# Kernel optimization log

Measured on AMD Instinct MI355X. Metric: run time of the kernel, lower is better.

The kernel has to match this reference:

```python
import jax, jax.numpy as jnp
import numpy as np

H, C = 2, 32  # heads, out_channels per head
NEG_SLOPE = 0.2


def gatv2_layer(h, src, dst, ea, W, b, We, att, bias, N):
    # shared lin_l = lin_r (share_weights=True)
    z = (h @ W + b).reshape(N, H, C)                      # [N,H,C]
    e = (ea @ We).reshape(-1, H, C)                        # [E',H,C]
    s = jax.nn.leaky_relu(z[dst] + z[src] + e, NEG_SLOPE)  # [E',H,C]
    alpha = jnp.einsum('ehc,hc->eh', s, att)               # [E',H]
    # segment softmax over destination neighborhoods
    m = jax.ops.segment_max(alpha, dst, num_segments=N)
    m = jnp.where(jnp.isfinite(m), m, 0.0)
    ex = jnp.exp(alpha - m[dst])
    denom = jax.ops.segment_sum(ex, dst, num_segments=N)
    a = ex / (denom[dst] + 1e-16)                          # [E',H]
    msg = (z[src] * a[:, :, None]).reshape(-1, H * C)      # [E',H*C]
    out = jax.ops.segment_sum(msg, dst, num_segments=N) + bias
    return out                                             # [N,H*C]


def setup_inputs() -> dict:
    key = jax.random.key(0)
    ks = jax.random.split(key, 16)
    N, E = 50000, 800000
    inp = {
        'x': jax.random.normal(ks[0], (N, 2), jnp.float32),
        'edge_index': jax.random.randint(ks[1], (2, E), 0, N, jnp.int64 if jax.config.jax_enable_x64 else jnp.int32).astype(jnp.int32),
        'edge_attr': jax.random.uniform(ks[2], (E, 2), jnp.float32),
        'dest_index': 123,
        'W0': jax.random.normal(ks[3], (2, 64), jnp.float32) * 0.5,
        'b0': jnp.zeros((64,), jnp.float32),
        'We0': jax.random.normal(ks[4], (2, 64), jnp.float32) * 0.5,
        'att0': jax.random.normal(ks[5], (H, C), jnp.float32) * 0.5,
        'bias0': jnp.zeros((64,), jnp.float32),
        'W1': jax.random.normal(ks[6], (64, 64), jnp.float32) * 0.125,
        'b1': jnp.zeros((64,), jnp.float32),
        'We1': jax.random.normal(ks[7], (2, 64), jnp.float32) * 0.5,
        'att1': jax.random.normal(ks[8], (H, C), jnp.float32) * 0.5,
        'bias1': jnp.zeros((64,), jnp.float32),
        'Wm1': jax.random.normal(ks[9], (194, 32), jnp.float32) * 0.07,
        'bm1': jnp.zeros((32,), jnp.float32),
        'Wm2': jax.random.normal(ks[10], (32, 1), jnp.float32) * 0.17,
        'bm2': jnp.zeros((1,), jnp.float32),
    }
    return inp


def reference(x, edge_index, edge_attr, dest_index,
              W0, b0, We0, att0, bias0,
              W1, b1, We1, att1, bias1,
              Wm1, bm1, Wm2, bm2):
    N = x.shape[0]
    # add self loops (fill_value='mean' for edge_attr)
    loops = jnp.arange(N, dtype=edge_index.dtype)
    src = jnp.concatenate([edge_index[0], loops])
    dst = jnp.concatenate([edge_index[1], loops])
    ea_sl = jnp.concatenate(
        [edge_attr, jnp.broadcast_to(edge_attr.mean(axis=0), (N, edge_attr.shape[1]))], axis=0)

    h = x
    h = jax.nn.elu(gatv2_layer(h, src, dst, ea_sl, W0, b0, We0, att0, bias0, N))
    h = jax.nn.elu(gatv2_layer(h, src, dst, ea_sl, W1, b1, We1, att1, bias1, N))

    goal = h[dest_index]                                   # [64]
    src_emb = h[edge_index[0]]                             # [E,64]
    dst_emb = h[edge_index[1]]                             # [E,64]
    goal_rep = jnp.broadcast_to(goal, (edge_index.shape[1], goal.shape[0]))
    edge_in = jnp.concatenate([src_emb, dst_emb, goal_rep, edge_attr], axis=-1)  # [E,194]
    hmlp = jax.nn.relu(edge_in @ Wm1 + bm1)
    logits = (hmlp @ Wm2 + bm2).squeeze(-1)                # [E]
    return logits
```

## Files before the change

### kernel.cpp

```cpp
#include <hip/hip_runtime.h>
#include <hip/hip_bf16.h>
#include <hip/hip_fp16.h>
#include <math.h>


typedef __attribute__((ext_vector_type(8))) short short8;
typedef __attribute__((ext_vector_type(4))) float f32x4;

#define BSH 6
#define CAP 2048
#define CH 4096

template <int IMM>
__device__ __forceinline__ float swz(float x) {
    return __int_as_float(__builtin_amdgcn_ds_swizzle(__float_as_int(x), IMM));
}

template <int CTRL>
__device__ __forceinline__ float dpp_add(float p) {
    int t = __builtin_amdgcn_update_dpp(0, __float_as_int(p), CTRL, 0xF, 0xF, true);
    return p + __int_as_float(t);
}

__device__ __forceinline__ short2 bsplit(float x) {
    unsigned u = __float_as_uint(x);
    short hi = (short)(u >> 16);
    float hif = __uint_as_float(u & 0xFFFF0000u);
    short lo = (short)(__float_as_uint(x - hif) >> 16);
    return make_short2(hi, lo);
}

__global__ __launch_bounds__(512) void setup_kernel(const float* __restrict__ W1,
                                                    const float* __restrict__ Wm1,
                                                    short* __restrict__ BfW1,
                                                    short* __restrict__ BfWm,
                                                    int* __restrict__ bucket_cursor,
                                                    float* __restrict__ easum, int nbuck) {
    if (blockIdx.x == 2) {
        for (int i = threadIdx.x; i < nbuck; i += 512) bucket_cursor[i] = i * CAP;
        if (threadIdx.x < 2) easum[threadIdx.x] = 0.f;
        return;
    }
    int snt = threadIdx.x >> 6;
    int lane = threadIdx.x & 63;
    int s = snt >> 2, nt = snt & 3;
    int col = nt * 16 + (lane & 15);
    short* Bf = blockIdx.x == 0 ? BfW1 : BfWm;
#pragma unroll
    for (int j = 0; j < 8; ++j) {
        int k = s * 32 + (lane >> 4) * 8 + j;
        float v;
        if (blockIdx.x == 0) {
            v = W1[k * 64 + col];
        } else {
            v = (col < 32) ? Wm1[k * 32 + col] : Wm1[(64 + k) * 32 + (col - 32)];
        }
        short2 t = bsplit(v);
        Bf[(snt * 2 + 0) * 512 + lane * 8 + j] = t.x;
        Bf[(snt * 2 + 1) * 512 + lane * 8 + j] = t.y;
    }
}

__global__ __launch_bounds__(256) void phaseA_kernel(const int* __restrict__ ei,
                                                     const float2* __restrict__ ea,
                                                     int* __restrict__ bucket_cursor,
                                                     float* __restrict__ easum,
                                                     float4* __restrict__ staged,
                                                     int E, int nbuck) {
    extern __shared__ int sm[];
    int* lcnt = sm;
    int* lbase = sm + nbuck;
    __shared__ float r0[4], r1[4];
    int tid = threadIdx.x;
    for (int i = tid; i < nbuck; i += 256) lcnt[i] = 0;
    __syncthreads();
    int base = blockIdx.x * CH;
    int end = min(base + CH, E);
    for (int i = base + tid; i < end; i += 256) {
        int d = ei[E + i];
        atomicAdd(&lcnt[d >> BSH], 1);
    }
    __syncthreads();
    for (int i = tid; i < nbuck; i += 256) {
        int c = lcnt[i];
        lbase[i] = c ? atomicAdd(&bucket_cursor[i], c) : 0;
        lcnt[i] = 0;
    }
    __syncthreads();
    float s0 = 0.f, s1 = 0.f;
    for (int i = base + tid; i < end; i += 256) {
        int s = ei[i], d = ei[E + i];
        float2 v = ea[i];
        s0 += v.x; s1 += v.y;
        int b = d >> BSH;
        int pos = lbase[b] + atomicAdd(&lcnt[b], 1);
        staged[pos] = make_float4(__int_as_float(s), v.x, v.y, __int_as_float(d));
    }
#pragma unroll
    for (int o = 32; o >= 1; o >>= 1) {
        s0 += __shfl_xor(s0, o);
        s1 += __shfl_xor(s1, o);
    }
    int wave = tid >> 6;
    if ((tid & 63) == 0) { r0[wave] = s0; r1[wave] = s1; }
    __syncthreads();
    if (tid == 0) {
        atomicAdd(&easum[0], r0[0] + r0[1] + r0[2] + r0[3]);
        atomicAdd(&easum[1], r1[0] + r1[1] + r1[2] + r1[3]);
    }
}

__global__ __launch_bounds__(512, 8) void phaseB_mega(
    const float4* __restrict__ staged, const int* __restrict__ bucket_cursor,
    const float* __restrict__ easum, const float2* __restrict__ x,
    const float* __restrict__ W0, const float* __restrict__ b0,
    const float* __restrict__ We, const float* __restrict__ att,
    const float* __restrict__ bias, const short* __restrict__ Bf,
    const float* __restrict__ b1,
    int* __restrict__ row_ptr, float4* __restrict__ recs,
    __half* __restrict__ z16, int N, int E, int nbuck) {
    __shared__ int cnt64[64];
    __shared__ int offs[64];
    __shared__ int psum8[8];
    __shared__ float acc6[64][6];
    __shared__ float h0s[64 * 64];
    int b = blockIdx.x;
    int n0g = b << BSH;
    int tid = threadIdx.x;
    int lane = tid & 63;
    int wave = tid >> 6;
    int local = 0;
    for (int j = tid; j < b; j += 512) local += bucket_cursor[j] - j * CAP;
#pragma unroll
    for (int o = 32; o >= 1; o >>= 1) local += __shfl_xor(local, o);
    if (tid < 64) cnt64[tid] = 0;
    for (int i = tid; i < 64 * 6; i += 512) ((float*)acc6)[i] = 0.f;
    if (lane == 0) psum8[wave] = local;
    __syncthreads();
    int bbase = 64 * b + psum8[0] + psum8[1] + psum8[2] + psum8[3]
                       + psum8[4] + psum8[5] + psum8[6] + psum8[7];
    int sbeg = b * CAP;
    int send = bucket_cursor[b];
    int nsl = send - sbeg;
    int nodes_here = min(64, N - n0g);
    int nrec = nsl + nodes_here;
    float invE = 1.f / (float)E;
    float m0 = easum[0] * invE, m1 = easum[1] * invE;

    {
        int sub = lane & 15;
        int eslot = lane >> 4;
        int ch0 = ((sub & 7) << 2) + ((sub >> 3) << 5);
        float Wx[4], Wy[4], bc[4], w0e[4], w1e[4], at[4];
#pragma unroll
        for (int j = 0; j < 4; ++j) {
            Wx[j] = W0[ch0 + j];  Wy[j] = W0[64 + ch0 + j];  bc[j] = b0[ch0 + j];
            w0e[j] = We[ch0 + j]; w1e[j] = We[64 + ch0 + j]; at[j] = att[ch0 + j];
        }
        int npass = (nsl + 3) >> 2;
        for (int p = wave; p < npass; p += 8) {
            int idx = p * 4 + eslot;
            bool valid = idx < nsl;
            float4 r = staged[sbeg + (valid ? idx : nsl - 1)];
            int s = __float_as_int(r.x);
            int d = __float_as_int(r.w);
            float2 xs = x[s];
            float2 xd = x[d];
            float P = 0.f;
#pragma unroll
            for (int j = 0; j < 4; ++j) {
                float zs = fmaf(xs.x, Wx[j], fmaf(xs.y, Wy[j], bc[j]));
                float zd = fmaf(xd.x, Wx[j], fmaf(xd.y, Wy[j], bc[j]));
                float t0 = zd + zs + fmaf(r.y, w0e[j], r.z * w1e[j]);
                t0 = fmaxf(t0, 0.2f * t0);
                P = fmaf(t0, at[j], P);
            }
            P += swz<0x041F>(P);
            P += swz<0x081F>(P);
            P += swz<0x101F>(P);
            float Po = swz<0x201F>(P);
            float Ph0 = (sub < 8) ? P : Po;
            float Ph1 = (sub < 8) ? Po : P;
            float w0 = __expf(fminf(Ph0, 60.f));
            float w1 = __expf(fminf(Ph1, 60.f));
            if (sub == 0 && valid) {
                int dl = d - n0g;
                atomicAdd(&acc6[dl][0], w0);
                atomicAdd(&acc6[dl][1], w0 * xs.x);
                atomicAdd(&acc6[dl][2], w0 * xs.y);
                atomicAdd(&acc6[dl][3], w1);
                atomicAdd(&acc6[dl][4], w1 * xs.x);
                atomicAdd(&acc6[dl][5], w1 * xs.y);
                atomicAdd(&cnt64[dl], 1);
            }
        }
    }
    __syncthreads();

    if (wave == 0) {
        int node = n0g + lane;
        int tot = cnt64[lane] + ((node < N) ? 1 : 0);
        int v = tot;
#pragma unroll
        for (int st = 1; st < 64; st <<= 1) {
            int u = __shfl_up(v, st);
            if (lane >= st) v += u;
        }
        if (node < N) {
            int excl = bbase + v - tot;
            row_ptr[node] = excl;
            recs[excl] = make_float4(__int_as_float(node), m0, m1, __int_as_float(node));
            offs[lane] = excl + 1;
        }
        if (b == nbuck - 1 && lane == 0) row_ptr[N] = bbase + nrec;
    }
    for (int k = 0; k < 8; ++k) {
        int q = wave + 8 * k;
        int ch = lane;
        int node = n0g + q;
        float hv = 0.f;
        if (node < N) {
            float2 xn = x[node];
            float W0c = W0[ch], W0c2 = W0[64 + ch], b0c = b0[ch];
            float zn = fmaf(xn.x, W0c, fmaf(xn.y, W0c2, b0c));
            float ts = fmaf(2.f, zn, fmaf(m0, We[ch], m1 * We[64 + ch]));
            ts = fmaxf(ts, 0.2f * ts);
            float p = ts * att[ch];
#pragma unroll
            for (int o = 1; o <= 16; o <<= 1) p += __shfl_xor(p, o);
            float wself = __expf(fminf(p, 60.f));
            int hsel = (ch >= 32) ? 3 : 0;
            float l  = acc6[q][hsel]     + wself;
            float Sx = acc6[q][hsel + 1] + wself * xn.x;
            float Sy = acc6[q][hsel + 2] + wself * xn.y;
            float num = fmaf(W0c, Sx, fmaf(W0c2, Sy, b0c * l));
            float v = num / (l + 1e-16f) + bias[ch];
            hv = (v > 0.f) ? v : expm1f(v);
        }
        h0s[q * 64 + ch] = hv;
    }
    __syncthreads();

    int m = lane & 15, quad = lane >> 4;
    int rowb = (wave & 3) * 16 + m;
    int ntb = (wave >> 2) * 2;
    f32x4 acc[2] = {{0.f, 0.f, 0.f, 0.f}, {0.f, 0.f, 0.f, 0.f}};
#pragma unroll
    for (int s = 0; s < 2; ++s) {
        const float* ap = h0s + rowb * 64 + s * 32 + quad * 8;
        float4 a0 = *(const float4*)ap;
        float4 a1 = *(const float4*)(ap + 4);
        short8 ahi, alo;
        short2 t;
        t = bsplit(a0.x); ahi[0] = t.x; alo[0] = t.y;
        t = bsplit(a0.y); ahi[1] = t.x; alo[1] = t.y;
        t = bsplit(a0.z); ahi[2] = t.x; alo[2] = t.y;
        t = bsplit(a0.w); ahi[3] = t.x; alo[3] = t.y;
        t = bsplit(a1.x); ahi[4] = t.x; alo[4] = t.y;
        t = bsplit(a1.y); ahi[5] = t.x; alo[5] = t.y;
        t = bsplit(a1.z); ahi[6] = t.x; alo[6] = t.y;
        t = bsplit(a1.w); ahi[7] = t.x; alo[7] = t.y;
#pragma unroll
        for (int u = 0; u < 2; ++u) {
            const short* bp = Bf + ((s * 4 + ntb + u) * 2) * 512 + lane * 8;
            short8 bhi = *(const short8*)bp;
            short8 blo = *(const short8*)(bp + 512);
            acc[u] = __builtin_amdgcn_mfma_f32_16x16x32_bf16(ahi, bhi, acc[u], 0, 0, 0);
            acc[u] = __builtin_amdgcn_mfma_f32_16x16x32_bf16(ahi, blo, acc[u], 0, 0, 0);
            acc[u] = __builtin_amdgcn_mfma_f32_16x16x32_bf16(alo, bhi, acc[u], 0, 0, 0);
        }
    }
#pragma unroll
    for (int u = 0; u < 2; ++u) {
        int col = (ntb + u) * 16 + m;
        float bj = b1[col];
#pragma unroll
        for (int r = 0; r < 4; ++r) {
            int orow = n0g + (wave & 3) * 16 + quad * 4 + r;
            if (orow < N) z16[(size_t)orow * 64 + col] = __float2half(acc[u][r] + bj);
        }
    }
    for (int i = sbeg + tid; i < send; i += 512) {
        float4 r = staged[i];
        int d = __float_as_int(r.w);
        int pos = atomicAdd(&offs[d - n0g], 1);
        recs[pos] = r;
    }
}

__global__ __launch_bounds__(256) void agg1_kernel(
    const __half* __restrict__ z, const int* __restrict__ row_ptr,
    const float4* __restrict__ recs,
    const float* __restrict__ We, const float* __restrict__ att,
    const float* __restrict__ bias, float* __restrict__ hout, int N) {
    int gtid = blockIdx.x * blockDim.x + threadIdx.x;
    int n = gtid >> 6;
    if (n >= N) return;
    n = __builtin_amdgcn_readfirstlane(n);
    int lane = threadIdx.x & 63;
    int half = lane >> 5;
    int c = (lane & 31) * 2;

    float We0a = We[c],      We0b = We[c + 1];
    float We1a = We[64 + c], We1b = We[64 + c + 1];
    float atta = att[c],     attb = att[c + 1];
    float2 znf = __half22float2(*(const __half2*)(z + (size_t)n * 64 + c));

    int beg = row_ptr[n], end = row_ptr[n + 1];
    float ll[4] = {0.f, 0.f, 0.f, 0.f};
    float a0[4] = {0.f, 0.f, 0.f, 0.f};
    float a1[4] = {0.f, 0.f, 0.f, 0.f};
    for (int i = beg; i < end; i += 8) {
        float w[4]; float2 zs[4];
#pragma unroll
        for (int k = 0; k < 4; ++k) {
            int idx = i + 2 * k + half;
            int idc = idx < end ? idx : end - 1;
            float4 r = recs[idc];
            int s = __float_as_int(r.x);
            zs[k] = __half22float2(*(const __half2*)(z + (size_t)s * 64 + c));
            float sj0 = znf.x + zs[k].x + fmaf(r.y, We0a, r.z * We1a);
            float sj1 = znf.y + zs[k].y + fmaf(r.y, We0b, r.z * We1b);
            sj0 = fmaxf(sj0, 0.2f * sj0);
            sj1 = fmaxf(sj1, 0.2f * sj1);
            float p = fmaf(sj0, atta, sj1 * attb);
            p = dpp_add<0xB1>(p);
            p = dpp_add<0x4E>(p);
            p = dpp_add<0x141>(p);
            p = dpp_add<0x140>(p);
            float ww = __expf(fminf(p, 60.f));
            w[k] = (idx < end) ? ww : 0.f;
        }
#pragma unroll
        for (int k = 0; k < 4; ++k) {
            ll[k] += w[k];
            a0[k] = fmaf(w[k], zs[k].x, a0[k]);
            a1[k] = fmaf(w[k], zs[k].y, a1[k]);
        }
    }
    float l  = (ll[0] + ll[1]) + (ll[2] + ll[3]);
    float s0 = (a0[0] + a0[1]) + (a0[2] + a0[3]);
    float s1 = (a1[0] + a1[1]) + (a1[2] + a1[3]);
    l  += __shfl_xor(l, 32);
    s0 += __shfl_xor(s0, 32);
    s1 += __shfl_xor(s1, 32);
    float inv = 1.f / (l + 1e-16f);
    float v0 = s0 * inv + bias[c];
    float v1 = s1 * inv + bias[c + 1];
    v0 = (v0 > 0.f) ? v0 : expm1f(v0);
    v1 = (v1 > 0.f) ? v1 : expm1f(v1);
    *(float2*)(hout + (size_t)n * 64 + c) = make_float2(v0, v1);
}

__global__ __launch_bounds__(256) void mfma_gemm64(const float* __restrict__ h,
                                                   const short* __restrict__ Bf,
                                                   __half* __restrict__ out, int N,
                                                   const float* __restrict__ Wm1,
                                                   const float* __restrict__ bm1,
                                                   const int* __restrict__ dest,
                                                   float* __restrict__ gv) {
    int wave = threadIdx.x >> 6;
    int lane = threadIdx.x & 63;
    int n0 = blockIdx.x * 64 + wave * 16;
    if (n0 < N) {
        int m = lane & 15, quad = lane >> 4;
        int arow = n0 + m;
        if (arow > N - 1) arow = N - 1;
        f32x4 acc[4] = {{0.f, 0.f, 0.f, 0.f}, {0.f, 0.f, 0.f, 0.f},
                        {0.f, 0.f, 0.f, 0.f}, {0.f, 0.f, 0.f, 0.f}};
#pragma unroll
        for (int s = 0; s < 2; ++s) {
            const float* ap = h + (size_t)arow * 64 + s * 32 + quad * 8;
            float4 a0 = *(const float4*)ap;
            float4 a1 = *(const float4*)(ap + 4);
            short8 ahi, alo;
            short2 t;
            t = bsplit(a0.x); ahi[0] = t.x; alo[0] = t.y;
            t = bsplit(a0.y); ahi[1] = t.x; alo[1] = t.y;
            t = bsplit(a0.z); ahi[2] = t.x; alo[2] = t.y;
            t = bsplit(a0.w); ahi[3] = t.x; alo[3] = t.y;
            t = bsplit(a1.x); ahi[4] = t.x; alo[4] = t.y;
            t = bsplit(a1.y); ahi[5] = t.x; alo[5] = t.y;
            t = bsplit(a1.z); ahi[6] = t.x; alo[6] = t.y;
            t = bsplit(a1.w); ahi[7] = t.x; alo[7] = t.y;
#pragma unroll
            for (int nt = 0; nt < 4; ++nt) {
                const short* bp = Bf + ((s * 4 + nt) * 2) * 512 + lane * 8;
                short8 bhi = *(const short8*)bp;
                short8 blo = *(const short8*)(bp + 512);
                acc[nt] = __builtin_amdgcn_mfma_f32_16x16x32_bf16(ahi, bhi, acc[nt], 0, 0, 0);
                acc[nt] = __builtin_amdgcn_mfma_f32_16x16x32_bf16(ahi, blo, acc[nt], 0, 0, 0);
                acc[nt] = __builtin_amdgcn_mfma_f32_16x16x32_bf16(alo, bhi, acc[nt], 0, 0, 0);
            }
        }
#pragma unroll
        for (int nt = 0; nt < 4; ++nt) {
            int col = nt * 16 + m;
#pragma unroll
            for (int r = 0; r < 4; ++r) {
                int orow = n0 + quad * 4 + r;
                if (orow < N) out[(size_t)orow * 64 + col] = __float2half(acc[nt][r]);
            }
        }
    }
    if (gv && blockIdx.x == 0 && threadIdx.x < 32) {
        int dd = dest[0];
        int q = threadIdx.x;
        float acc2 = bm1[q];
        for (int k = 0; k < 64; ++k)
            acc2 = fmaf(h[(size_t)dd * 64 + k], Wm1[(128 + k) * 32 + q], acc2);
        gv[q] = acc2;
    }
}

__global__ __launch_bounds__(256) void edge_mlp_kernel(
    const int* __restrict__ ei, const float2* __restrict__ ea,
    const __half* __restrict__ hsd, const float* __restrict__ gvec,
    const float* __restrict__ WrowA, const float* __restrict__ WrowB,
    const float* __restrict__ Wm2, const float* __restrict__ bm2,
    float* __restrict__ out, int E) {
    int tid = blockIdx.x * blockDim.x + threadIdx.x;
    int e = tid >> 3;
    int j = tid & 7;
    if (e >= E) return;
    int s = ei[e], d = ei[E + e];
    float2 eav = ea[e];
    const __half2* ps = (const __half2*)(hsd + (size_t)s * 64 + j * 4);
    const __half2* pd = (const __half2*)(hsd + (size_t)d * 64 + 32 + j * 4);
    float2 a01 = __half22float2(ps[0]), a23 = __half22float2(ps[1]);
    float2 b01 = __half22float2(pd[0]), b23 = __half22float2(pd[1]);
    float4 g = *(const float4*)(gvec + j * 4);
    float4 wa = *(const float4*)(WrowA + j * 4);
    float4 wb = *(const float4*)(WrowB + j * 4);
    float4 w2 = *(const float4*)(Wm2 + j * 4);
    float acc = 0.f, v;
    v = fmaf(eav.x, wa.x, fmaf(eav.y, wb.x, a01.x + b01.x + g.x)); v = fmaxf(v, 0.f); acc = fmaf(v, w2.x, acc);
    v = fmaf(eav.x, wa.y, fmaf(eav.y, wb.y, a01.y + b01.y + g.y)); v = fmaxf(v, 0.f); acc = fmaf(v, w2.y, acc);
    v = fmaf(eav.x, wa.z, fmaf(eav.y, wb.z, a23.x + b23.x + g.z)); v = fmaxf(v, 0.f); acc = fmaf(v, w2.z, acc);
    v = fmaf(eav.x, wa.w, fmaf(eav.y, wb.w, a23.y + b23.y + g.w)); v = fmaxf(v, 0.f); acc = fmaf(v, w2.w, acc);
    acc = dpp_add<0xB1>(acc);
    acc = dpp_add<0x4E>(acc);
    acc = dpp_add<0x141>(acc);
    if (j == 0) out[e] = acc + bm2[0];
}

extern "C" void kernel_launch(void* const* d_in, const int* in_sizes, int n_in,
                              void* d_out, int out_size, void* d_ws, size_t ws_size,
                              hipStream_t stream) {
    const float* x     = (const float*)d_in[0];
    const int*   ei    = (const int*)d_in[1];
    const float* ea    = (const float*)d_in[2];
    const int*   dest  = (const int*)d_in[3];
    const float* W0    = (const float*)d_in[4];
    const float* b0    = (const float*)d_in[5];
    const float* We0   = (const float*)d_in[6];
    const float* att0  = (const float*)d_in[7];
    const float* bias0 = (const float*)d_in[8];
    const float* W1    = (const float*)d_in[9];
    const float* b1    = (const float*)d_in[10];
    const float* We1   = (const float*)d_in[11];
    const float* att1  = (const float*)d_in[12];
    const float* bias1 = (const float*)d_in[13];
    const float* Wm1   = (const float*)d_in[14];
    const float* bm1   = (const float*)d_in[15];
    const float* Wm2   = (const float*)d_in[16];
    const float* bm2   = (const float*)d_in[17];

    const int N = in_sizes[0] / 2;
    const int E = in_sizes[1] / 2;
    const int nbuck = (N + 63) >> BSH;
    const int nchunk = (E + CH - 1) / CH;

    char* ws = (char*)d_ws;
    size_t off = 0;
    auto alloc = [&](size_t bytes) -> void* {
        void* p = ws + off;
        off += bytes;
        off = (off + 255) & ~(size_t)255;
        return p;
    };
    int*    bucket_cursor = (int*)alloc((size_t)nbuck * 4);
    int*    row_ptr       = (int*)alloc((size_t)(N + 1) * 4);
    size_t  slack_bytes   = (size_t)nbuck * CAP * 16;
    float4* staged        = (float4*)alloc(slack_bytes);
    float4* recs          = (float4*)alloc((size_t)(E + N) * 16);
    __half* z16           = (__half*)alloc((size_t)N * 64 * 2);
    float*  hbuf          = (float*)alloc((size_t)N * 64 * 4);
    float*  easum         = (float*)alloc(8);
    float*  gvec          = (float*)alloc(32 * 4);
    short*  BfW1          = (short*)alloc(8192 * 2);
    short*  BfWm          = (short*)alloc(8192 * 2);
    __half* hsd16         = z16;

    dim3 blk(256);
    setup_kernel<<<3, 512, 0, stream>>>(W1, Wm1, BfW1, BfWm, bucket_cursor, easum, nbuck);
    phaseA_kernel<<<nchunk, blk, (size_t)nbuck * 8, stream>>>(ei, (const float2*)ea,
                                                              bucket_cursor, easum,
                                                              staged, E, nbuck);
    phaseB_mega<<<nbuck, 512, 0, stream>>>(staged, bucket_cursor, easum,
                                           (const float2*)x, W0, b0, We0, att0, bias0,
                                           BfW1, b1, row_ptr, recs, z16, N, E, nbuck);
    agg1_kernel<<<(N * 64 + 255) / 256, blk, 0, stream>>>(z16, row_ptr, recs,
                                                          We1, att1, bias1, hbuf, N);
    mfma_gemm64<<<(N + 63) / 64, blk, 0, stream>>>(hbuf, BfWm, hsd16, N,
                                                   Wm1, bm1, dest, gvec);
    edge_mlp_kernel<<<((size_t)E * 8 + 255) / 256, blk, 0, stream>>>(
        ei, (const float2*)ea, hsd16, gvec,
        Wm1 + 192 * 32, Wm1 + 193 * 32, Wm2, bm2, (float*)d_out, E);
}
```

Before: 255.8 us.

## Move layer-0 edge attention scoring into the bucketing pass with per-edge weights

```diff
diff --git a/kernel.cpp b/kernel.cpp
--- a/kernel.cpp
+++ b/kernel.cpp
@@ -9,12 +9,7 @@
 
 #define BSH 6
 #define CAP 2048
-#define CH 4096
-
-template <int IMM>
-__device__ __forceinline__ float swz(float x) {
-    return __int_as_float(__builtin_amdgcn_ds_swizzle(__float_as_int(x), IMM));
-}
+#define CH 1024
 
 template <int CTRL>
 __device__ __forceinline__ float dpp_add(float p) {
@@ -35,9 +30,12 @@
                                                     short* __restrict__ BfW1,
                                                     short* __restrict__ BfWm,
                                                     int* __restrict__ bucket_cursor,
-                                                    float* __restrict__ easum, int nbuck) {
+                                                    float* __restrict__ easum,
+                                                    int* __restrict__ gcnt,
+                                                    int nbuck, int N) {
     if (blockIdx.x == 2) {
         for (int i = threadIdx.x; i < nbuck; i += 512) bucket_cursor[i] = i * CAP;
+        for (int i = threadIdx.x; i < N; i += 512) gcnt[i] = 0;
         if (threadIdx.x < 2) easum[threadIdx.x] = 0.f;
         return;
     }
@@ -63,15 +61,28 @@
 
 __global__ __launch_bounds__(256) void phaseA_kernel(const int* __restrict__ ei,
                                                      const float2* __restrict__ ea,
+                                                     const float2* __restrict__ x,
+                                                     const float* __restrict__ W0,
+                                                     const float* __restrict__ b0,
+                                                     const float* __restrict__ We,
+                                                     const float* __restrict__ att,
                                                      int* __restrict__ bucket_cursor,
                                                      float* __restrict__ easum,
+                                                     int* __restrict__ gcnt,
                                                      float4* __restrict__ staged,
+                                                     float4* __restrict__ wstaged,
                                                      int E, int nbuck) {
     extern __shared__ int sm[];
     int* lcnt = sm;
     int* lbase = sm + nbuck;
+    __shared__ float4 wpA[64];
+    __shared__ float2 wpB[64];
     __shared__ float r0[4], r1[4];
     int tid = threadIdx.x;
+    if (tid < 64) {
+        wpA[tid] = make_float4(W0[tid], W0[64 + tid], We[tid], We[64 + tid]);
+        wpB[tid] = make_float2(2.f * b0[tid], att[tid]);
+    }
     for (int i = tid; i < nbuck; i += 256) lcnt[i] = 0;
     __syncthreads();
     int base = blockIdx.x * CH;
@@ -92,9 +103,30 @@
         int s = ei[i], d = ei[E + i];
         float2 v = ea[i];
         s0 += v.x; s1 += v.y;
+        float2 xs = x[s], xd = x[d];
+        float sx = xs.x + xd.x, sy = xs.y + xd.y;
+        float P0 = 0.f, P1 = 0.f;
+#pragma unroll 8
+        for (int c = 0; c < 32; ++c) {
+            float4 a = wpA[c]; float2 bb = wpB[c];
+            float t = fmaf(sx, a.x, fmaf(sy, a.y, fmaf(v.x, a.z, fmaf(v.y, a.w, bb.x))));
+            t = fmaxf(t, 0.2f * t);
+            P0 = fmaf(t, bb.y, P0);
+        }
+#pragma unroll 8
+        for (int c = 32; c < 64; ++c) {
+            float4 a = wpA[c]; float2 bb = wpB[c];
+            float t = fmaf(sx, a.x, fmaf(sy, a.y, fmaf(v.x, a.z, fmaf(v.y, a.w, bb.x))));
+            t = fmaxf(t, 0.2f * t);
+            P1 = fmaf(t, bb.y, P1);
+        }
+        float w0 = __expf(fminf(P0, 60.f));
+        float w1 = __expf(fminf(P1, 60.f));
         int b = d >> BSH;
         int pos = lbase[b] + atomicAdd(&lcnt[b], 1);
         staged[pos] = make_float4(__int_as_float(s), v.x, v.y, __int_as_float(d));
+        wstaged[pos] = make_float4(w0, w1, xs.x, xs.y);
+        atomicAdd(&gcnt[d], 1);
     }
 #pragma unroll
     for (int o = 32; o >= 1; o >>= 1) {
@@ -111,7 +143,8 @@
 }
 
 __global__ __launch_bounds__(512, 8) void phaseB_mega(
-    const float4* __restrict__ staged, const int* __restrict__ bucket_cursor,
+    const float4* __restrict__ staged, const float4* __restrict__ wstaged,
+    const int* __restrict__ bucket_cursor, const int* __restrict__ gcnt,
     const float* __restrict__ easum, const float2* __restrict__ x,
     const float* __restrict__ W0, const float* __restrict__ b0,
     const float* __restrict__ We, const float* __restrict__ att,
@@ -119,10 +152,9 @@
     const float* __restrict__ b1,
     int* __restrict__ row_ptr, float4* __restrict__ recs,
     __half* __restrict__ z16, int N, int E, int nbuck) {
-    __shared__ int cnt64[64];
     __shared__ int offs[64];
     __shared__ int psum8[8];
-    __shared__ float acc6[64][6];
+    __shared__ float acc7[64][7];
     __shared__ float h0s[64 * 64];
     int b = blockIdx.x;
     int n0g = b << BSH;
@@ -133,8 +165,7 @@
     for (int j = tid; j < b; j += 512) local += bucket_cursor[j] - j * CAP;
 #pragma unroll
     for (int o = 32; o >= 1; o >>= 1) local += __shfl_xor(local, o);
-    if (tid < 64) cnt64[tid] = 0;
-    for (int i = tid; i < 64 * 6; i += 512) ((float*)acc6)[i] = 0.f;
+    for (int i = tid; i < 64 * 7; i += 512) ((float*)acc7)[i] = 0.f;
     if (lane == 0) psum8[wave] = local;
     __syncthreads();
     int bbase = 64 * b + psum8[0] + psum8[1] + psum8[2] + psum8[3]
@@ -147,59 +178,10 @@
     float invE = 1.f / (float)E;
     float m0 = easum[0] * invE, m1 = easum[1] * invE;
 
-    {
-        int sub = lane & 15;
-        int eslot = lane >> 4;
-        int ch0 = ((sub & 7) << 2) + ((sub >> 3) << 5);
-        float Wx[4], Wy[4], bc[4], w0e[4], w1e[4], at[4];
-#pragma unroll
-        for (int j = 0; j < 4; ++j) {
-            Wx[j] = W0[ch0 + j];  Wy[j] = W0[64 + ch0 + j];  bc[j] = b0[ch0 + j];
-            w0e[j] = We[ch0 + j]; w1e[j] = We[64 + ch0 + j]; at[j] = att[ch0 + j];
-        }
-        int npass = (nsl + 3) >> 2;
-        for (int p = wave; p < npass; p += 8) {
-            int idx = p * 4 + eslot;
-            bool valid = idx < nsl;
-            float4 r = staged[sbeg + (valid ? idx : nsl - 1)];
-            int s = __float_as_int(r.x);
-            int d = __float_as_int(r.w);
-            float2 xs = x[s];
-            float2 xd = x[d];
-            float P = 0.f;
-#pragma unroll
-            for (int j = 0; j < 4; ++j) {
-                float zs = fmaf(xs.x, Wx[j], fmaf(xs.y, Wy[j], bc[j]));
-                float zd = fmaf(xd.x, Wx[j], fmaf(xd.y, Wy[j], bc[j]));
-                float t0 = zd + zs + fmaf(r.y, w0e[j], r.z * w1e[j]);
-                t0 = fmaxf(t0, 0.2f * t0);
-                P = fmaf(t0, at[j], P);
-            }
-            P += swz<0x041F>(P);
-            P += swz<0x081F>(P);
-            P += swz<0x101F>(P);
-            float Po = swz<0x201F>(P);
-            float Ph0 = (sub < 8) ? P : Po;
-            float Ph1 = (sub < 8) ? Po : P;
-            float w0 = __expf(fminf(Ph0, 60.f));
-            float w1 = __expf(fminf(Ph1, 60.f));
-            if (sub == 0 && valid) {
-                int dl = d - n0g;
-                atomicAdd(&acc6[dl][0], w0);
-                atomicAdd(&acc6[dl][1], w0 * xs.x);
-                atomicAdd(&acc6[dl][2], w0 * xs.y);
-                atomicAdd(&acc6[dl][3], w1);
-                atomicAdd(&acc6[dl][4], w1 * xs.x);
-                atomicAdd(&acc6[dl][5], w1 * xs.y);
-                atomicAdd(&cnt64[dl], 1);
-            }
-        }
-    }
-    __syncthreads();
-
     if (wave == 0) {
         int node = n0g + lane;
-        int tot = cnt64[lane] + ((node < N) ? 1 : 0);
+        int cnt = (node < N) ? gcnt[node] : 0;
+        int tot = cnt + ((node < N) ? 1 : 0);
         int v = tot;
 #pragma unroll
         for (int st = 1; st < 64; st <<= 1) {
@@ -214,6 +196,24 @@
         }
         if (b == nbuck - 1 && lane == 0) row_ptr[N] = bbase + nrec;
     }
+    __syncthreads();
+
+    for (int i = sbeg + tid; i < send; i += 512) {
+        float4 r = staged[i];
+        float4 wv = wstaged[i];
+        int d = __float_as_int(r.w);
+        int dl = d - n0g;
+        atomicAdd(&acc7[dl][0], wv.x);
+        atomicAdd(&acc7[dl][1], wv.x * wv.z);
+        atomicAdd(&acc7[dl][2], wv.x * wv.w);
+        atomicAdd(&acc7[dl][3], wv.y);
+        atomicAdd(&acc7[dl][4], wv.y * wv.z);
+        atomicAdd(&acc7[dl][5], wv.y * wv.w);
+        int pos = atomicAdd(&offs[dl], 1);
+        recs[pos] = r;
+    }
+    __syncthreads();
+
     for (int k = 0; k < 8; ++k) {
         int q = wave + 8 * k;
         int ch = lane;
@@ -230,9 +230,9 @@
             for (int o = 1; o <= 16; o <<= 1) p += __shfl_xor(p, o);
             float wself = __expf(fminf(p, 60.f));
             int hsel = (ch >= 32) ? 3 : 0;
-            float l  = acc6[q][hsel]     + wself;
-            float Sx = acc6[q][hsel + 1] + wself * xn.x;
-            float Sy = acc6[q][hsel + 2] + wself * xn.y;
+            float l  = acc7[q][hsel]     + wself;
+            float Sx = acc7[q][hsel + 1] + wself * xn.x;
+            float Sy = acc7[q][hsel + 2] + wself * xn.y;
             float num = fmaf(W0c, Sx, fmaf(W0c2, Sy, b0c * l));
             float v = num / (l + 1e-16f) + bias[ch];
             hv = (v > 0.f) ? v : expm1f(v);
@@ -279,12 +279,6 @@
             int orow = n0g + (wave & 3) * 16 + quad * 4 + r;
             if (orow < N) z16[(size_t)orow * 64 + col] = __float2half(acc[u][r] + bj);
         }
-    }
-    for (int i = sbeg + tid; i < send; i += 512) {
-        float4 r = staged[i];
-        int d = __float_as_int(r.w);
-        int pos = atomicAdd(&offs[d - n0g], 1);
-        recs[pos] = r;
     }
 }
 
@@ -483,23 +477,27 @@
     int*    row_ptr       = (int*)alloc((size_t)(N + 1) * 4);
     size_t  slack_bytes   = (size_t)nbuck * CAP * 16;
     float4* staged        = (float4*)alloc(slack_bytes);
+    float4* wstaged       = (float4*)alloc(slack_bytes);
     float4* recs          = (float4*)alloc((size_t)(E + N) * 16);
     __half* z16           = (__half*)alloc((size_t)N * 64 * 2);
     float*  hbuf          = (float*)alloc((size_t)N * 64 * 4);
     float*  easum         = (float*)alloc(8);
     float*  gvec          = (float*)alloc(32 * 4);
+    int*    gcnt          = (int*)alloc((size_t)N * 4);
     short*  BfW1          = (short*)alloc(8192 * 2);
     short*  BfWm          = (short*)alloc(8192 * 2);
     __half* hsd16         = z16;
 
     dim3 blk(256);
-    setup_kernel<<<3, 512, 0, stream>>>(W1, Wm1, BfW1, BfWm, bucket_cursor, easum, nbuck);
-    phaseA_kernel<<<nchunk, blk, (size_t)nbuck * 8, stream>>>(ei, (const float2*)ea,
-                                                              bucket_cursor, easum,
-                                                              staged, E, nbuck);
-    phaseB_mega<<<nbuck, 512, 0, stream>>>(staged, bucket_cursor, easum,
-                                           (const float2*)x, W0, b0, We0, att0, bias0,
-                                           BfW1, b1, row_ptr, recs, z16, N, E, nbuck);
+    setup_kernel<<<3, 512, 0, stream>>>(W1, Wm1, BfW1, BfWm, bucket_cursor,
+                                        easum, gcnt, nbuck, N);
+    phaseA_kernel<<<nchunk, blk, (size_t)nbuck * 8, stream>>>(
+        ei, (const float2*)ea, (const float2*)x, W0, b0, We0, att0,
+        bucket_cursor, easum, gcnt, staged, wstaged, E, nbuck);
+    phaseB_mega<<<nbuck, 512, 0, stream>>>(staged, wstaged, bucket_cursor, gcnt,
+                                           easum, (const float2*)x, W0, b0, We0,
+                                           att0, bias0, BfW1, b1, row_ptr, recs,
+                                           z16, N, E, nbuck);
     agg1_kernel<<<(N * 64 + 255) / 256, blk, 0, stream>>>(z16, row_ptr, recs,
                                                           We1, att1, bias1, hbuf, N);
     mfma_gemm64<<<(N + 63) / 64, blk, 0, stream>>>(hbuf, BfWm, hsd16, N,
```

Result: slower. 294.6 us (+15.2%).
